# Performance work log

Hardware: AMD Instinct MI355X
Metric: run time of the kernel (lower is better)

## Reference

```python
import jax, jax.numpy as jnp
import numpy as np

_CONTRACTION_EPS = 0.002


def setup_inputs() -> dict:
    key = jax.random.key(0)
    k_u, k_s, k_k = jax.random.split(key, 3)
    B, T, d_in, d_out, d_x = 16, 2048, 512, 512, 512
    u = jax.random.normal(k_u, (B, T, d_in), dtype=jnp.float32)
    state = jnp.zeros((B, d_x), dtype=jnp.float32)
    # mirror init_orthogonal_spectrum: S = I + 0.01 * randn (well-conditioned)
    S = jnp.eye(d_x, dtype=jnp.float32) + 0.01 * jax.random.normal(k_s, (d_x, d_x), dtype=jnp.float32)
    K_raw = jax.random.normal(k_k, (d_x + d_out, d_x + d_in), dtype=jnp.float32)
    log_gamma = jnp.array(0.0, dtype=jnp.float32)  # gamma = 1.0
    return {"u": u, "state": state, "S": S, "K_raw": K_raw, "log_gamma": log_gamma}


def _ssm_matrices(S, K_raw, log_gamma, d_x):
    # contraction: K = K_raw / (sigma_max(K_raw) + eps)
    sigma = jnp.maximum(jnp.linalg.svd(K_raw, compute_uv=False)[0], 1e-5)
    K = K_raw / (sigma + _CONTRACTION_EPS)
    K11 = K[:d_x, :d_x]
    K12 = K[:d_x, d_x:]
    K21 = K[d_x:, :d_x]
    K22 = K[d_x:, d_x:]
    Sinv = jnp.linalg.inv(S)
    gamma = jnp.exp(log_gamma)
    A = Sinv @ K11 @ S
    Bm = gamma * (Sinv @ K12)
    C = K21 @ S
    D = gamma * K22
    return A, Bm, C, D


def reference(u, state, S, K_raw, log_gamma):
    # u: (B, T, d_in), state: (B, d_x)
    d_x = state.shape[1]
    A, Bm, C, D = _ssm_matrices(S, K_raw, log_gamma, d_x)
    At, Bt = A.T, Bm.T

    def step(x, u_t):
        # x_{t+1} = x A^T + u_t B^T ; emit pre-update state x_t
        x_next = x @ At + u_t @ Bt
        return x_next, x

    x_last, pre = jax.lax.scan(step, state, jnp.swapaxes(u, 0, 1))
    pre = jnp.swapaxes(pre, 0, 1)                      # (B, T, d_x) = states[:, :-1]
    states = jnp.concatenate([pre, x_last[:, None, :]], axis=1)  # (B, T+1, d_x)
    # y_t = C x_t + D u_t, vectorized over time
    output = pre @ C.T + u @ D.T                       # (B, T, d_out)
    return output, states
```

## Files before the change

kernel.cpp:

```cpp
#include <hip/hip_runtime.h>
#include <string.h>

typedef _Float16 f16x8 __attribute__((ext_vector_type(8)));
typedef _Float16 f16x4 __attribute__((ext_vector_type(4)));
typedef __fp16   hf2   __attribute__((ext_vector_type(2)));
typedef float    f32x4 __attribute__((ext_vector_type(4)));

struct Addr { long hi; long lo; int sh; int msk; };

__device__ __forceinline__ long raddr(const Addr a, int r) {
  return ((long)(r >> a.sh)) * a.hi + ((long)(r & a.msk)) * a.lo;
}

struct GP {
  int M, N, K1, K2;
  const float* A1; Addr a1;
  const float* A2; Addr a2;
  const _Float16* Bh; int ldbh;
  const float* scale;
  float alpha;
  const float* E1; Addr e1; float beta;
  float* C1; Addr c1;
  _Float16* C1h; int ldh;
  float* C2; Addr c2;
  const float* E2; Addr e2;
  const float* fin;
  float* fout;
};

struct GPB { GP g[10]; };

__device__ __forceinline__ f16x4 pk4s(f32x4 v, float ss) {
  hf2 lo = __builtin_amdgcn_cvt_pkrtz(v[0] * ss, v[1] * ss);
  hf2 hi = __builtin_amdgcn_cvt_pkrtz(v[2] * ss, v[3] * ss);
  f16x4 h;
  h[0] = (_Float16)lo[0]; h[1] = (_Float16)lo[1];
  h[2] = (_Float16)hi[0]; h[3] = (_Float16)hi[1];
  return h;
}

template<int BM, bool DEEP>
__device__ __forceinline__ void gemm_body(const GP& p) {
  constexpr int BN = BM;
  constexpr int WT = BM / 2;
  constexpr int FM = WT / 16;
  constexpr int NAQ = BM / 32;
  constexpr int NBH = BN / 64;
  __shared__ _Float16 As[BM * 40];
  __shared__ _Float16 Bs[BN * 40];
  __shared__ float red[256];
  const int tid = threadIdx.x;
  const int nbn = (p.N + BN - 1) / BN;
  const int nbm = (p.M + BM - 1) / BM;
  if ((int)blockIdx.x >= nbm * nbn) return;
  int bm, bn;
  {
    const int bid = blockIdx.x;
    if ((nbm & 7) == 0) {
      bm = (bid & 7) + ((bid >> 3) / nbn) * 8;
      bn = (bid >> 3) % nbn;
    } else {
      bm = bid / nbn; bn = bid - bm * nbn;
    }
  }
  const int m0 = bm * BM, n0 = bn * BN;

  float sscale = 1.0f;
  if (p.fin) {
    red[tid] = p.fin[tid];
    __syncthreads();
    for (int st = 128; st > 0; st >>= 1) {
      if (tid < st) red[tid] += red[tid + st];
      __syncthreads();
    }
    sscale = 1.0f / sqrtf(red[0]);
    __syncthreads();
  }
  float alpha = p.alpha;
  if (p.scale) alpha *= p.scale[0];
  if (p.fin) alpha *= sscale;

  const int w = tid >> 6, l = tid & 63;
  const int wm = w >> 1, wn = w & 1;
  const int lr = l & 15, lg = l >> 4;

  f32x4 acc[FM][FM];
  #pragma unroll
  for (int m = 0; m < FM; ++m)
    #pragma unroll
    for (int n = 0; n < FM; ++n) acc[m][n] = {0.f, 0.f, 0.f, 0.f};

  const int Kt = p.K1 + p.K2;

  f32x4 aR0[NAQ], aR1[NAQ];
  f16x8 b2R0[NBH], b2R1[NBH];

  auto loadT = [&](int k0, f32x4* aR, f16x8* b2R) {
    const float* Ab; Addr aa; long kl;
    if (k0 < p.K1) { Ab = p.A1; aa = p.a1; kl = k0; }
    else           { Ab = p.A2; aa = p.a2; kl = (long)k0 - p.K1; }
    #pragma unroll
    for (int i = 0; i < NAQ; ++i) {
      const int gq = tid + (i << 8);
      const int ar_ = gq >> 3, kq = gq & 7;
      f32x4 v = {0.f, 0.f, 0.f, 0.f};
      if (m0 + ar_ < p.M) v = *(const f32x4*)(Ab + raddr(aa, m0 + ar_) + kl + kq * 4);
      aR[i] = v;
    }
    #pragma unroll
    for (int i = 0; i < NBH; ++i) {
      const int row = (tid >> 2) + i * 64;
      b2R[i] = *(const f16x8*)(p.Bh + (long)(n0 + row) * p.ldbh + k0 + (tid & 3) * 8);
    }
  };
  auto storeLDS = [&](const f32x4* aR, const f16x8* b2R) {
    #pragma unroll
    for (int i = 0; i < NAQ; ++i) {
      const int gq = tid + (i << 8);
      const int ar_ = gq >> 3, kq = gq & 7;
      *(f16x4*)&As[ar_ * 40 + kq * 4] = pk4s(aR[i], sscale);
    }
    #pragma unroll
    for (int i = 0; i < NBH; ++i) {
      const int row = (tid >> 2) + i * 64;
      *(f16x8*)&Bs[row * 40 + (tid & 3) * 8] = b2R[i];
    }
  };
  auto compute = [&]() {
    f16x8 a[FM], b[FM];
    #pragma unroll
    for (int m = 0; m < FM; ++m)
      a[m] = *(const f16x8*)&As[(wm * WT + m * 16 + lr) * 40 + lg * 8];
    #pragma unroll
    for (int n = 0; n < FM; ++n)
      b[n] = *(const f16x8*)&Bs[(wn * WT + n * 16 + lr) * 40 + lg * 8];
    #pragma unroll
    for (int m = 0; m < FM; ++m)
      #pragma unroll
      for (int n = 0; n < FM; ++n)
        acc[m][n] = __builtin_amdgcn_mfma_f32_16x16x32_f16(a[m], b[n], acc[m][n], 0, 0, 0);
  };

  if constexpr (DEEP) {
    f32x4 aRC[NAQ];
    f16x8 bRC[NBH];
    loadT(0, aR0, b2R0);
    if (Kt > 32) loadT(32, aR1, b2R1);
    for (int k0 = 0; k0 < Kt; k0 += 32) {
      if (k0 + 64 < Kt) loadT(k0 + 64, aRC, bRC);
      storeLDS(aR0, b2R0);
      __syncthreads();
      compute();
      __syncthreads();
      #pragma unroll
      for (int i = 0; i < NAQ; ++i) aR0[i] = aR1[i];
      #pragma unroll
      for (int i = 0; i < NBH; ++i) b2R0[i] = b2R1[i];
      #pragma unroll
      for (int i = 0; i < NAQ; ++i) aR1[i] = aRC[i];
      #pragma unroll
      for (int i = 0; i < NBH; ++i) b2R1[i] = bRC[i];
    }
  } else {
    loadT(0, aR0, b2R0);
    for (int k0 = 0; k0 < Kt; k0 += 64) {
      storeLDS(aR0, b2R0);
      __syncthreads();
      loadT(k0 + 32, aR1, b2R1);
      compute();
      __syncthreads();
      storeLDS(aR1, b2R1);
      __syncthreads();
      if (k0 + 64 < Kt) loadT(k0 + 64, aR0, b2R0);
      compute();
      __syncthreads();
    }
  }

  float ssq = 0.0f;
  #pragma unroll
  for (int m = 0; m < FM; ++m) {
    #pragma unroll
    for (int n = 0; n < FM; ++n) {
      #pragma unroll
      for (int rr = 0; rr < 4; ++rr) {
        const int ro = m0 + wm * WT + m * 16 + lg * 4 + rr;
        const int no = n0 + wn * WT + n * 16 + lr;
        if (ro < p.M) {
          float val = alpha * acc[m][n][rr];
          float o1 = val;
          if (p.E1) o1 += p.beta * p.E1[raddr(p.e1, ro) + no];
          if (p.C1) p.C1[raddr(p.c1, ro) + no] = o1;
          if (p.C1h) p.C1h[(long)no * p.ldh + ro] = (_Float16)o1;
          if (p.C2) p.C2[raddr(p.c2, ro) + no] = val + p.E2[raddr(p.e2, ro) + no];
          ssq += val * val;
        }
      }
    }
  }
  if (p.fout) {
    __syncthreads();
    red[tid] = ssq;
    __syncthreads();
    for (int st = 128; st > 0; st >>= 1) {
      if (tid < st) red[tid] += red[tid + st];
      __syncthreads();
    }
    if (tid == 0) p.fout[blockIdx.x] = red[0];
  }
}

__global__ __launch_bounds__(256) void gemm_u64(GPB pb)  { gemm_body<64, true>(pb.g[blockIdx.y]); }
__global__ __launch_bounds__(256) void gemm_u128(GPB pb) { gemm_body<128, false>(pb.g[blockIdx.y]); }

__global__ void prep1_k(const float* S, const float* Kr, const float* st0,
                        float* Krt, _Float16* KrH, float* St, float* Xa,
                        _Float16* XaH, float* Za,
                        float* K11u, float* K12u, _Float16* K21uH) {
  const int op = blockIdx.y;
  const int tx = threadIdx.x, ty = threadIdx.y;
  const int lid = ty * 32 + tx;
  if (op == 4) {
    if (blockIdx.x >= 256) return;
    const int base = (blockIdx.x * 256 + lid) * 4;
    #pragma unroll
    for (int q = 0; q < 4; ++q) {
      const int e = base + q;
      const int i = e >> 9, j = e & 511;
      XaH[e] = (_Float16)(((i == j) ? 2.0f : 0.0f) - S[(long)i * 512 + j]);
    }
    return;
  }
  if (op == 5) {
    if (blockIdx.x >= 32) return;
    const int idx = blockIdx.x * 256 + lid;
    const int b = idx >> 9, j = idx & 511;
    Za[(long)b * 262144 + j] = st0[idx];
    return;
  }
  if (op == 8) {
    if (blockIdx.x >= 256) return;
    const int base = (blockIdx.x * 256 + lid) * 4;
    #pragma unroll
    for (int q = 0; q < 4; ++q) {
      const int e = base + q;
      const int n = e >> 9, k = e & 511;
      K21uH[e] = (_Float16)Kr[(long)(512 + n) * 1024 + k];
    }
    return;
  }
  __shared__ float t[32][33];
  if (op <= 1) {
    if (blockIdx.x >= 1024) return;
    const int bx = blockIdx.x & 31, by = blockIdx.x >> 5;
    const long I0 = (long)bx * 32, J0 = (long)by * 32;
    #pragma unroll
    for (int k = 0; k < 4; ++k)
      t[ty * 4 + k][tx] = Kr[(J0 + ty * 4 + k) * 1024 + I0 + tx];
    __syncthreads();
    #pragma unroll
    for (int k = 0; k < 4; ++k) {
      const long i = I0 + ty * 4 + k, j = J0 + tx;
      if (op == 0) Krt[i * 1024 + j] = t[tx][ty * 4 + k];
      else         KrH[i * 1024 + j] = (_Float16)t[tx][ty * 4 + k];
    }
  } else {
    if (blockIdx.x >= 256) return;
    const int bx = blockIdx.x & 15, by = blockIdx.x >> 4;
    const long I0 = (long)bx * 32, J0 = (long)by * 32;
    const float* src;
    long ld, coff;
    if (op == 6) { src = Kr; ld = 1024; coff = 0; }
    else if (op == 7) { src = Kr; ld = 1024; coff = 512; }
    else { src = S; ld = 512; coff = 0; }
    #pragma unroll
    for (int k = 0; k < 4; ++k)
      t[ty * 4 + k][tx] = src[(J0 + ty * 4 + k) * ld + coff + I0 + tx];
    __syncthreads();
    #pragma unroll
    for (int k = 0; k < 4; ++k) {
      const long i = I0 + ty * 4 + k, j = J0 + tx;
      if (op == 2) St[i * 512 + j] = t[tx][ty * 4 + k];
      else if (op == 3) Xa[i * 512 + j] = ((i == j) ? 2.0f : 0.0f) - t[tx][ty * 4 + k];
      else if (op == 6) K11u[i * 512 + j] = t[tx][ty * 4 + k];
      else K12u[i * 512 + j] = t[tx][ty * 4 + k];
    }
  }
}

__global__ void prep2_k(const float* Kr, const float* sc, _Float16* ABstH,
                        _Float16* StackH, const _Float16* BtuH,
                        _Float16* CtDtH, float* APf2) {
  const int op = blockIdx.y;
  const int lid = threadIdx.y * 32 + threadIdx.x;
  const float invk = sc[0], gik = sc[2];
  const float ik2 = invk * invk, ik2g = ik2 * sc[1];
  if (op == 0) {
    if (blockIdx.x >= 512) return;
    const int base = (blockIdx.x * 256 + lid) * 4;
    #pragma unroll
    for (int q = 0; q < 4; ++q) {
      const int e = base + q;
      const int n = e >> 10, c = e & 1023;
      if (c < 512) ABstH[e] = (_Float16)((float)ABstH[e] * invk);
      else ABstH[e] = (_Float16)(gik * (float)BtuH[(long)n * 512 + (c - 512)]);
    }
  } else if (op == 1) {
    if (blockIdx.x >= 768) return;
    const int base = (blockIdx.x * 256 + lid) * 4;
    #pragma unroll
    for (int q = 0; q < 4; ++q) {
      const int e = base + q;
      const int n = e / 1536, c = e - n * 1536;
      float v;
      if (c < 512) v = (float)StackH[e] * ik2;
      else if (c < 1024) v = (float)StackH[e] * ik2g;
      else v = gik * (float)BtuH[(long)n * 512 + (c - 1024)];
      StackH[e] = (_Float16)v;
    }
  } else if (op == 2) {
    if (blockIdx.x >= 512) return;
    const int base = (blockIdx.x * 256 + lid) * 4;
    #pragma unroll
    for (int q = 0; q < 4; ++q) {
      const int e = base + q;
      const int n = e >> 10, c = e & 1023;
      if (c < 512) CtDtH[e] = (_Float16)((float)CtDtH[e] * invk);
      else CtDtH[e] = (_Float16)(gik * Kr[(long)(512 + n) * 1024 + 512 + (c - 512)]);
    }
  } else {
    if (blockIdx.x >= 256) return;
    const int base = (blockIdx.x * 256 + lid) * 4;
    #pragma unroll
    for (int q = 0; q < 4; ++q) APf2[base + q] *= ik2;
  }
}

__global__ void scalar_k(const float* P, int nsq, const float* lg, float* sc) {
  __shared__ float red[256];
  __shared__ float sv[16];
  const int tid = threadIdx.x;
  for (int k = 0; k <= nsq; ++k) {
    red[tid] = P[k * 256 + tid];
    __syncthreads();
    for (int st = 128; st > 0; st >>= 1) {
      if (tid < st) red[tid] += red[tid + st];
      __syncthreads();
    }
    if (tid == 0) sv[k] = red[0];
    __syncthreads();
  }
  if (tid != 0) return;
  double lnl = 0.0, wgt = 1.0;
  for (int k = 0; k <= nsq; ++k) {
    double sk = sqrt((double)sv[k]);
    lnl += wgt * log(sk);
    if (k < nsq) wgt *= 0.5;
  }
  double sigma = exp(0.5 * lnl);
  if (sigma < 1e-5) sigma = 1e-5;
  const double invk = 1.0 / (sigma + 0.002);
  const double g = exp((double)lg[0]);
  sc[0] = (float)invk;
  sc[1] = (float)g;
  sc[2] = (float)(g * invk);
}

static inline Addr lin(long stride) {
  Addr a; a.hi = 0; a.lo = stride; a.sh = 20; a.msk = 0xFFFFF; return a;
}
static inline Addr two(int sh, long hi, int msk, long lo) {
  Addr a; a.hi = hi; a.lo = lo; a.sh = sh; a.msk = msk; return a;
}
static inline GP gp0() {
  GP p; memset(&p, 0, sizeof(p)); p.alpha = 1.0f; p.beta = 1.0f; return p;
}

extern "C" void kernel_launch(void* const* d_in, const int* in_sizes, int n_in,
                              void* d_out, int out_size, void* d_ws, size_t ws_size,
                              hipStream_t stream) {
  (void)in_sizes; (void)n_in; (void)out_size; (void)ws_size;
  const float* u    = (const float*)d_in[0];
  const float* st0  = (const float*)d_in[1];
  const float* S    = (const float*)d_in[2];
  const float* Kr   = (const float*)d_in[3];
  const float* lgam = (const float*)d_in[4];

  float* outp   = (float*)d_out;
  float* states = outp + (long)16 * 2048 * 512;
  float* ws = (float*)d_ws;

  const int NSQ = 8;
  float* sc = ws;
  float* P  = ws + 64;
  float* base = ws + 3456;

  float* Krt = base;
  _Float16* MbH = (_Float16*)base;
  float* Ma  = base + 1048576;
  float* Mb  = base + 2097152;
  _Float16* CtDtH  = (_Float16*)(ws + 3149248);
  _Float16* MaH    = (_Float16*)(ws + 3419584);
  _Float16* StackH = (_Float16*)(ws + 3943872);
  _Float16* zerosH = (_Float16*)(ws + 4337088);

  float* Za  = outp;
  float* Zb  = outp + 4194304;
  float* APb = outp + 8388608;
  float* Tb  = outp + 10223616;
  float* K11u = Tb;
  float* K12u = Tb + 262144;
  float* AtU  = Tb + 524288;
  float* BtU  = Tb + 786432;
  _Float16* h16   = (_Float16*)(outp + 12320768);
  _Float16* ABstH = h16;
  _Float16* APH_  = h16 + 524288;
  _Float16* TmH_  = h16 + 2097152;
  _Float16* XaH   = h16 + 4194304;
  _Float16* XbH   = XaH + 262144;
  _Float16* YnH   = XbH + 262144;
  _Float16* WH    = YnH + 262144;
  _Float16* K21uH = WH + 262144;
  _Float16* KrH   = K21uH + 262144;
  _Float16* BtuH  = h16 + 6553600;
  float* St = outp + 15728640;
  float* Xa = outp + 15990784;
  float* Xb = outp + 16252928;
  float* Yn = outp + 16515072;

  auto APf = [&](int j) -> float* {
    return APb + (long)(j - 2) * 262144;
  };
  auto APHp = [&](int j) -> const _Float16* {
    if (j == 1) return ABstH;
    if (j == 2) return StackH;
    return APH_ + (long)(j - 3) * 262144;
  };
  auto APHl = [&](int j) { return (j == 1) ? 1024 : ((j == 2) ? 1536 : 512); };
  auto Tmf = [&](int k) -> float* { return (k == 0) ? APf(8) : Tb + (long)(k - 1) * 262144; };
  auto TmH = [&](int k) -> _Float16* {
    return (k == 0) ? (_Float16*)APHp(8) : TmH_ + (long)(k - 1) * 262144;
  };

  auto launch64 = [&](const GP* gs, int nb) {
    GPB pb; memset(&pb, 0, sizeof(pb));
    int mx = 0;
    for (int i = 0; i < nb; ++i) {
      pb.g[i] = gs[i];
      int b = ((gs[i].M + 63) / 64) * ((gs[i].N + 63) / 64);
      if (b > mx) mx = b;
    }
    gemm_u64<<<dim3(mx, nb), dim3(256), 0, stream>>>(pb);
  };
  auto launch128 = [&](const GP* gs, int nb) {
    GPB pb; memset(&pb, 0, sizeof(pb));
    int mx = 0;
    for (int i = 0; i < nb; ++i) {
      pb.g[i] = gs[i];
      int b = ((gs[i].M + 127) / 128) * ((gs[i].N + 127) / 128);
      if (b > mx) mx = b;
    }
    gemm_u128<<<dim3(mx, nb), dim3(256), 0, stream>>>(pb);
  };

  auto mmh = [&](const float* A, const _Float16* Bh, int ldbh,
                 float* C, _Float16* Ch, int ldh) {
    GP g = gp0(); g.M = 512; g.N = 512; g.K1 = 512;
    g.A1 = A; g.a1 = lin(512);
    g.Bh = Bh; g.ldbh = ldbh;
    g.C1 = C; g.c1 = lin(512);
    g.C1h = Ch; g.ldh = ldh;
    return g;
  };
  auto cpGP = [&](const float* src, Addr sa, float* dst, Addr da, int M) {
    GP g = gp0(); g.M = M; g.N = 512; g.K1 = 64;
    g.A1 = src; g.a1 = sa;
    g.Bh = zerosH; g.ldbh = 64;
    g.E1 = src; g.e1 = sa; g.beta = 1.0f;
    g.C1 = dst; g.c1 = da;
    return g;
  };

  hipMemsetAsync(zerosH, 0, 512 * 64 * sizeof(_Float16), stream);
  prep1_k<<<dim3(1024, 9), dim3(32, 8), 0, stream>>>(S, Kr, st0, Krt, KrH,
                                                     St, Xa, XaH, Za,
                                                     K11u, K12u, K21uH);

  {
    GP gs[2];
    gs[0] = gp0();
    gs[0].M = 1024; gs[0].N = 1024; gs[0].K1 = 1024;
    gs[0].A1 = Krt; gs[0].a1 = lin(1024);
    gs[0].Bh = KrH; gs[0].ldbh = 1024;
    gs[0].C1 = Ma; gs[0].c1 = lin(1024);
    gs[0].C1h = MaH; gs[0].ldh = 1024;
    gs[0].fout = P;
    gs[1] = mmh(St, XaH, 512, Yn, YnH, 512);
    launch64(gs, 2);
  }
  for (int k = 1; k <= NSQ; ++k) {
    const bool odd = (k % 2 == 1);
    float* cur = odd ? Ma : Mb;
    float* nxt = odd ? Mb : Ma;
    _Float16* curH = odd ? MaH : MbH;
    _Float16* nxtH = odd ? MbH : MaH;
    GP gs[3];
    gs[0] = gp0();
    gs[0].M = 1024; gs[0].N = 1024; gs[0].K1 = 1024;
    gs[0].A1 = cur; gs[0].a1 = lin(1024);
    gs[0].Bh = curH; gs[0].ldbh = 1024;
    gs[0].C1 = nxt; gs[0].c1 = lin(1024);
    gs[0].C1h = nxtH; gs[0].ldh = 1024;
    gs[0].fin = P + (long)(k - 1) * 256;
    gs[0].fout = P + (long)k * 256;
    int nb = 1;
    if (k <= 5) {
      if (odd) {
        float* cx = (k == 1 || k == 5) ? Xa : Xb;
        float* nx = (k == 1 || k == 5) ? Xb : Xa;
        _Float16* nxH = (k == 1 || k == 5) ? XbH : XaH;
        GP h = mmh(cx, YnH, 512, nx, nxH, 512);
        h.alpha = -1.0f; h.E1 = cx; h.e1 = lin(512); h.beta = 2.0f;
        gs[nb++] = h;
      } else {
        _Float16* cxH = (k == 2) ? XbH : XaH;
        gs[nb++] = mmh(St, cxH, 512, Yn, YnH, 512);
      }
    } else if (k == 6) {
      gs[nb++] = mmh(K11u, XbH, 512, nullptr, WH, 512);
      gs[nb++] = mmh(St, K21uH, 512, nullptr, CtDtH, 1024);
    } else if (k == 7) {
      gs[nb++] = mmh(St, WH, 512, AtU, ABstH, 1024);
      gs[nb++] = mmh(K12u, XbH, 512, BtU, BtuH, 512);
    } else {
      gs[nb++] = mmh(AtU, ABstH, 1024, APf(2), StackH, 1536);
      gs[nb++] = mmh(BtU, ABstH, 1024, nullptr, StackH + 512, 1536);
    }
    launch64(gs, nb);
  }
  scalar_k<<<1, 256, 0, stream>>>(P, NSQ, lgam, sc);
  prep2_k<<<dim3(768, 4), dim3(32, 8), 0, stream>>>(Kr, sc, ABstH, StackH,
                                                    BtuH, CtDtH, APf(2));

  const Addr A_u8   = two(8, 1048576, 255, 4096);
  const Addr A_s8   = two(8, 1049088, 255, 4096);
  const Addr A_z    = two(8, 262144, 255, 512);
  const Addr A_srow = two(11, 1049088, 2047, 512);

  for (int j = 2; j <= 8; j += 2) {
    GP gs[5];
    int nb = 0;
    GP m = gp0();
    m.M = 4096; m.N = 512;
    if (j == 2) {
      m.K1 = 1024; m.A1 = u; m.a1 = A_u8;
      m.Bh = StackH + 512; m.ldbh = 1536;
    } else {
      m.K1 = 512; m.A1 = states + (long)(j - 2) * 512; m.a1 = A_s8;
      m.K2 = 1024; m.A2 = u + (long)(j - 2) * 512; m.a2 = A_u8;
      m.Bh = StackH; m.ldbh = 1536;
    }
    if (j == 8) { m.C1 = Za + 512; m.c1 = A_z; }
    else { m.C1 = states + (long)j * 512; m.c1 = A_s8; }
    gs[nb++] = m;
    if (j == 2) {
      gs[nb++] = mmh(APf(2), ABstH, 1024, APf(3), APH_ + 0, 512);
      gs[nb++] = mmh(APf(2), StackH, 1536, APf(4), APH_ + 262144, 512);
    } else if (j == 4) {
      for (int i = 1; i <= 4; ++i)
        gs[nb++] = mmh(APf(4), APHp(i), APHl(i), APf(4 + i),
                       APH_ + (long)(i + 1) * 262144, 512);
    } else if (j == 6) {
      gs[nb++] = mmh(Tmf(0), TmH(0), 512, Tmf(1), TmH(1), 512);
    } else {
      gs[nb++] = mmh(Tmf(1), TmH(1), 512, Tmf(2), TmH(2), 512);
    }
    launch64(gs, nb);
  }

  for (int k = 0; k <= 2; ++k) {
    const int s = 1 << k;
    float* Zs = (k % 2 == 0) ? Za : Zb;
    float* Zd = (k % 2 == 0) ? Zb : Za;
    GP gs[7];
    int nb = 0;
    GP m = gp0();
    m.M = 4096; m.N = 512; m.K1 = 512;
    m.A1 = Zs; m.a1 = A_z;
    m.Bh = TmH(k); m.ldbh = 512;
    m.E1 = Zs + (long)s * 512; m.e1 = A_z; m.beta = 1.0f;
    m.C1 = Zd + (long)s * 512; m.c1 = A_z;
    gs[nb++] = m;
    const Addr lowA = two(k, 262144, s - 1, 512);
    gs[nb++] = cpGP(Zs, lowA, Zd, lowA, 16 * s);
    if (k == 0) {
      for (int j = 1; j <= 7; j += 2) {
        GP g = gp0();
        g.M = 4096; g.N = 512;
        if (j == 1) {
          g.K1 = 512; g.A1 = u; g.a1 = A_u8;
          g.Bh = ABstH + 512; g.ldbh = 1024;
        } else {
          g.K1 = 512; g.A1 = states + (long)(j - 1) * 512; g.a1 = A_s8;
          g.K2 = 512; g.A2 = u + (long)(j - 1) * 512; g.a2 = A_u8;
          g.Bh = ABstH; g.ldbh = 1024;
        }
        g.C1 = states + (long)j * 512; g.c1 = A_s8;
        gs[nb++] = g;
      }
    }
    launch64(gs, nb);
  }
  float* Zf = Zb;

  {
    GP gs[9];
    for (int j = 1; j <= 7; ++j) {
      GP g = gp0();
      g.M = 4096; g.N = 512; g.K1 = 512;
      g.A1 = Zf; g.a1 = A_z;
      g.Bh = APHp(j); g.ldbh = APHl(j);
      g.C2 = states + (long)j * 512; g.c2 = A_s8;
      g.E2 = states + (long)j * 512; g.e2 = A_s8;
      gs[j - 1] = g;
    }
    gs[7] = cpGP(Zf, A_z, states, A_s8, 4096);
    gs[8] = cpGP(Zf + (long)256 * 512, lin(262144),
                 states + (long)2048 * 512, lin(1049088), 16);
    launch128(gs, 9);
  }

  {
    GP g = gp0();
    g.M = 32768; g.N = 512;
    g.K1 = 512; g.A1 = states; g.a1 = A_srow;
    g.K2 = 512; g.A2 = u; g.a2 = lin(512);
    g.Bh = CtDtH; g.ldbh = 1024;
    g.C1 = outp; g.c1 = lin(512);
    launch128(&g, 1);
  }
}
```

Baseline: 581.6 us.

## Restructure chunked scan schedule with 4-step stack and fold scalar kernel into prep2

Adds a 4-step stacked input matrix (A^3B, A^2B, AB, B scaled by powers of the contraction factor) so the intra-chunk state recurrence jumps directly from states[0] to states[4] and then to the chunk end. It regroups the batched GEMM launches across the log-depth Z scan so independent state GEMMs run alongside the scan stages, cutting the number of dependent launches. It also merges the scalar reduction kernel into prep2 (every block recomputes sigma) and replaces a memset with a prep1 op. In exchange there is more redundant reduction work per block, a larger K=2048 GEMM, and buffer aliasing (BtAtU on Tb, Stack4H over Xa) that must not collide with live data.

```diff
diff --git a/kernel.cpp b/kernel.cpp
--- a/kernel.cpp
+++ b/kernel.cpp
@@ -216,7 +216,8 @@
 __global__ void prep1_k(const float* S, const float* Kr, const float* st0,
                         float* Krt, _Float16* KrH, float* St, float* Xa,
                         _Float16* XaH, float* Za,
-                        float* K11u, float* K12u, _Float16* K21uH) {
+                        float* K11u, float* K12u, _Float16* K21uH,
+                        _Float16* zerosH) {
   const int op = blockIdx.y;
   const int tx = threadIdx.x, ty = threadIdx.y;
   const int lid = ty * 32 + tx;
@@ -247,6 +248,12 @@
       const int n = e >> 9, k = e & 511;
       K21uH[e] = (_Float16)Kr[(long)(512 + n) * 1024 + k];
     }
+    return;
+  }
+  if (op == 9) {
+    if (blockIdx.x >= 32) return;
+    const int base = (blockIdx.x * 256 + lid);
+    *(f16x4*)&zerosH[base * 4] = f16x4{0, 0, 0, 0};
     return;
   }
   __shared__ float t[32][33];
@@ -288,13 +295,39 @@
   }
 }
 
-__global__ void prep2_k(const float* Kr, const float* sc, _Float16* ABstH,
-                        _Float16* StackH, const _Float16* BtuH,
-                        _Float16* CtDtH, float* APf2) {
+__global__ void prep2_k(const float* Kr, const float* P, const float* lg,
+                        _Float16* ABstH, _Float16* StackH,
+                        const _Float16* BtuH, _Float16* CtDtH, float* APf2,
+                        _Float16* Stack4H, const float* BtAtU) {
+  __shared__ float red[256];
+  __shared__ float sv[9];
+  const int lid = threadIdx.y * 32 + threadIdx.x;
+  for (int k = 0; k < 9; ++k) {
+    red[lid] = P[k * 256 + lid];
+    __syncthreads();
+    for (int st = 128; st > 0; st >>= 1) {
+      if (lid < st) red[lid] += red[lid + st];
+      __syncthreads();
+    }
+    if (lid == 0) sv[k] = red[0];
+    __syncthreads();
+  }
+  double lnl = 0.0, wgt = 1.0;
+  for (int k = 0; k < 9; ++k) {
+    lnl += wgt * log(sqrt((double)sv[k]));
+    if (k < 8) wgt *= 0.5;
+  }
+  double sigma = exp(0.5 * lnl);
+  if (sigma < 1e-5) sigma = 1e-5;
+  const float invk = (float)(1.0 / (sigma + 0.002));
+  const float gma  = (float)exp((double)lg[0]);
+  const float gik  = gma * invk;
+  const float ik2  = invk * invk;
+  const float ik2g = ik2 * gma;
+  const float ik3g = ik2 * invk * gma;
+  const float ik4g = ik2 * ik2 * gma;
+
   const int op = blockIdx.y;
-  const int lid = threadIdx.y * 32 + threadIdx.x;
-  const float invk = sc[0], gik = sc[2];
-  const float ik2 = invk * invk, ik2g = ik2 * sc[1];
   if (op == 0) {
     if (blockIdx.x >= 512) return;
     const int base = (blockIdx.x * 256 + lid) * 4;
@@ -328,42 +361,27 @@
       if (c < 512) CtDtH[e] = (_Float16)((float)CtDtH[e] * invk);
       else CtDtH[e] = (_Float16)(gik * Kr[(long)(512 + n) * 1024 + 512 + (c - 512)]);
     }
-  } else {
+  } else if (op == 3) {
     if (blockIdx.x >= 256) return;
     const int base = (blockIdx.x * 256 + lid) * 4;
     #pragma unroll
     for (int q = 0; q < 4; ++q) APf2[base + q] *= ik2;
-  }
-}
-
-__global__ void scalar_k(const float* P, int nsq, const float* lg, float* sc) {
-  __shared__ float red[256];
-  __shared__ float sv[16];
-  const int tid = threadIdx.x;
-  for (int k = 0; k <= nsq; ++k) {
-    red[tid] = P[k * 256 + tid];
-    __syncthreads();
-    for (int st = 128; st > 0; st >>= 1) {
-      if (tid < st) red[tid] += red[tid + st];
-      __syncthreads();
-    }
-    if (tid == 0) sv[k] = red[0];
-    __syncthreads();
-  }
-  if (tid != 0) return;
-  double lnl = 0.0, wgt = 1.0;
-  for (int k = 0; k <= nsq; ++k) {
-    double sk = sqrt((double)sv[k]);
-    lnl += wgt * log(sk);
-    if (k < nsq) wgt *= 0.5;
-  }
-  double sigma = exp(0.5 * lnl);
-  if (sigma < 1e-5) sigma = 1e-5;
-  const double invk = 1.0 / (sigma + 0.002);
-  const double g = exp((double)lg[0]);
-  sc[0] = (float)invk;
-  sc[1] = (float)g;
-  sc[2] = (float)(g * invk);
+  } else {
+    if (blockIdx.x >= 1024) return;
+    const int base = (blockIdx.x * 256 + lid) * 4;
+    #pragma unroll
+    for (int q = 0; q < 4; ++q) {
+      const int e = base + q;
+      const int n = e >> 11, c = e & 2047;
+      _Float16* dst = &Stack4H[(long)n * 2560 + 512 + c];
+      float v;
+      if (c < 512) v = (float)*dst * ik4g;
+      else if (c < 1024) v = (float)*dst * ik3g;
+      else if (c < 1536) v = ik2g * BtAtU[(long)(c - 1024) * 512 + n];
+      else v = gik * (float)BtuH[(long)n * 512 + (c - 1536)];
+      *dst = (_Float16)v;
+    }
+  }
 }
 
 static inline Addr lin(long stride) {
@@ -391,7 +409,6 @@
   float* ws = (float*)d_ws;
 
   const int NSQ = 8;
-  float* sc = ws;
   float* P  = ws + 64;
   float* base = ws + 3456;
 
@@ -408,10 +425,11 @@
   float* Zb  = outp + 4194304;
   float* APb = outp + 8388608;
   float* Tb  = outp + 10223616;
-  float* K11u = Tb;
-  float* K12u = Tb + 262144;
-  float* AtU  = Tb + 524288;
-  float* BtU  = Tb + 786432;
+  float* K11u  = Tb;
+  float* K12u  = Tb + 262144;
+  float* AtU   = Tb + 524288;
+  float* BtU   = Tb + 786432;
+  float* BtAtU = Tb;
   _Float16* h16   = (_Float16*)(outp + 12320768);
   _Float16* ABstH = h16;
   _Float16* APH_  = h16 + 524288;
@@ -427,6 +445,7 @@
   float* Xa = outp + 15990784;
   float* Xb = outp + 16252928;
   float* Yn = outp + 16515072;
+  _Float16* Stack4H = (_Float16*)(outp + 15990784);
 
   auto APf = [&](int j) -> float* {
     return APb + (long)(j - 2) * 262144;
@@ -434,9 +453,12 @@
   auto APHp = [&](int j) -> const _Float16* {
     if (j == 1) return ABstH;
     if (j == 2) return StackH;
+    if (j == 4) return Stack4H;
     return APH_ + (long)(j - 3) * 262144;
   };
-  auto APHl = [&](int j) { return (j == 1) ? 1024 : ((j == 2) ? 1536 : 512); };
+  auto APHl = [&](int j) {
+    return (j == 1) ? 1024 : ((j == 2) ? 1536 : ((j == 4) ? 2560 : 512));
+  };
   auto Tmf = [&](int k) -> float* { return (k == 0) ? APf(8) : Tb + (long)(k - 1) * 262144; };
   auto TmH = [&](int k) -> _Float16* {
     return (k == 0) ? (_Float16*)APHp(8) : TmH_ + (long)(k - 1) * 262144;
@@ -481,10 +503,9 @@
     return g;
   };
 
-  hipMemsetAsync(zerosH, 0, 512 * 64 * sizeof(_Float16), stream);
-  prep1_k<<<dim3(1024, 9), dim3(32, 8), 0, stream>>>(S, Kr, st0, Krt, KrH,
-                                                     St, Xa, XaH, Za,
-                                                     K11u, K12u, K21uH);
+  prep1_k<<<dim3(1024, 10), dim3(32, 8), 0, stream>>>(S, Kr, st0, Krt, KrH,
+                                                      St, Xa, XaH, Za,
+                                                      K11u, K12u, K21uH, zerosH);
 
   {
     GP gs[2];
@@ -534,55 +555,57 @@
       gs[nb++] = mmh(K12u, XbH, 512, BtU, BtuH, 512);
     } else {
       gs[nb++] = mmh(AtU, ABstH, 1024, APf(2), StackH, 1536);
-      gs[nb++] = mmh(BtU, ABstH, 1024, nullptr, StackH + 512, 1536);
+      gs[nb++] = mmh(BtU, ABstH, 1024, BtAtU, StackH + 512, 1536);
     }
     launch64(gs, nb);
   }
-  scalar_k<<<1, 256, 0, stream>>>(P, NSQ, lgam, sc);
-  prep2_k<<<dim3(768, 4), dim3(32, 8), 0, stream>>>(Kr, sc, ABstH, StackH,
-                                                    BtuH, CtDtH, APf(2));
+
+  {
+    GP gs[2];
+    gs[0] = mmh(BtAtU, ABstH, 1024, nullptr, Stack4H + 1024, 2560);
+    gs[1] = mmh(BtAtU, StackH, 1536, nullptr, Stack4H + 512, 2560);
+    launch64(gs, 2);
+  }
+  prep2_k<<<dim3(1024, 5), dim3(32, 8), 0, stream>>>(Kr, P, lgam, ABstH, StackH,
+                                                     BtuH, CtDtH, APf(2),
+                                                     Stack4H, BtAtU);
 
   const Addr A_u8   = two(8, 1048576, 255, 4096);
   const Addr A_s8   = two(8, 1049088, 255, 4096);
   const Addr A_z    = two(8, 262144, 255, 512);
   const Addr A_srow = two(11, 1049088, 2047, 512);
 
-  for (int j = 2; j <= 8; j += 2) {
+  {
+    GP gs[3];
+    gs[0] = gp0();
+    gs[0].M = 4096; gs[0].N = 512;
+    gs[0].K1 = 2048; gs[0].A1 = u; gs[0].a1 = A_u8;
+    gs[0].Bh = Stack4H + 512; gs[0].ldbh = 2560;
+    gs[0].C1 = states + (long)4 * 512; gs[0].c1 = A_s8;
+    gs[1] = mmh(APf(2), ABstH, 1024, nullptr, APH_ + 0, 512);
+    gs[2] = mmh(APf(2), StackH, 1536, APf(4), Stack4H, 2560);
+    launch64(gs, 3);
+  }
+  {
     GP gs[5];
-    int nb = 0;
-    GP m = gp0();
-    m.M = 4096; m.N = 512;
-    if (j == 2) {
-      m.K1 = 1024; m.A1 = u; m.a1 = A_u8;
-      m.Bh = StackH + 512; m.ldbh = 1536;
-    } else {
-      m.K1 = 512; m.A1 = states + (long)(j - 2) * 512; m.a1 = A_s8;
-      m.K2 = 1024; m.A2 = u + (long)(j - 2) * 512; m.a2 = A_u8;
-      m.Bh = StackH; m.ldbh = 1536;
-    }
-    if (j == 8) { m.C1 = Za + 512; m.c1 = A_z; }
-    else { m.C1 = states + (long)j * 512; m.c1 = A_s8; }
-    gs[nb++] = m;
-    if (j == 2) {
-      gs[nb++] = mmh(APf(2), ABstH, 1024, APf(3), APH_ + 0, 512);
-      gs[nb++] = mmh(APf(2), StackH, 1536, APf(4), APH_ + 262144, 512);
-    } else if (j == 4) {
-      for (int i = 1; i <= 4; ++i)
-        gs[nb++] = mmh(APf(4), APHp(i), APHl(i), APf(4 + i),
-                       APH_ + (long)(i + 1) * 262144, 512);
-    } else if (j == 6) {
-      gs[nb++] = mmh(Tmf(0), TmH(0), 512, Tmf(1), TmH(1), 512);
-    } else {
-      gs[nb++] = mmh(Tmf(1), TmH(1), 512, Tmf(2), TmH(2), 512);
-    }
-    launch64(gs, nb);
+    gs[0] = gp0();
+    gs[0].M = 4096; gs[0].N = 512;
+    gs[0].K1 = 512; gs[0].A1 = states + (long)4 * 512; gs[0].a1 = A_s8;
+    gs[0].K2 = 2048; gs[0].A2 = u + (long)4 * 512; gs[0].a2 = A_u8;
+    gs[0].Bh = Stack4H; gs[0].ldbh = 2560;
+    gs[0].C1 = Za + 512; gs[0].c1 = A_z;
+    gs[1] = mmh(APf(4), ABstH, 1024, nullptr, APH_ + 2 * 262144, 512);
+    gs[2] = mmh(APf(4), StackH, 1536, nullptr, APH_ + 3 * 262144, 512);
+    gs[3] = mmh(APf(4), APH_ + 0, 512, nullptr, APH_ + 4 * 262144, 512);
+    gs[4] = mmh(APf(4), Stack4H, 2560, APf(8), APH_ + 5 * 262144, 512);
+    launch64(gs, 5);
   }
 
   for (int k = 0; k <= 2; ++k) {
     const int s = 1 << k;
     float* Zs = (k % 2 == 0) ? Za : Zb;
     float* Zd = (k % 2 == 0) ? Zb : Za;
-    GP gs[7];
+    GP gs[8];
     int nb = 0;
     GP m = gp0();
     m.M = 4096; m.N = 512; m.K1 = 512;
@@ -594,20 +617,55 @@
     const Addr lowA = two(k, 262144, s - 1, 512);
     gs[nb++] = cpGP(Zs, lowA, Zd, lowA, 16 * s);
     if (k == 0) {
-      for (int j = 1; j <= 7; j += 2) {
-        GP g = gp0();
-        g.M = 4096; g.N = 512;
-        if (j == 1) {
-          g.K1 = 512; g.A1 = u; g.a1 = A_u8;
-          g.Bh = ABstH + 512; g.ldbh = 1024;
-        } else {
-          g.K1 = 512; g.A1 = states + (long)(j - 1) * 512; g.a1 = A_s8;
-          g.K2 = 512; g.A2 = u + (long)(j - 1) * 512; g.a2 = A_u8;
-          g.Bh = ABstH; g.ldbh = 1024;
-        }
-        g.C1 = states + (long)j * 512; g.c1 = A_s8;
+      {
+        GP g = gp0(); g.M = 4096; g.N = 512;
+        g.K1 = 512; g.A1 = u; g.a1 = A_u8;
+        g.Bh = ABstH + 512; g.ldbh = 1024;
+        g.C1 = states + (long)1 * 512; g.c1 = A_s8;
         gs[nb++] = g;
       }
+      {
+        GP g = gp0(); g.M = 4096; g.N = 512;
+        g.K1 = 1024; g.A1 = u; g.a1 = A_u8;
+        g.Bh = StackH + 512; g.ldbh = 1536;
+        g.C1 = states + (long)2 * 512; g.c1 = A_s8;
+        gs[nb++] = g;
+      }
+      {
+        GP g = gp0(); g.M = 4096; g.N = 512;
+        g.K1 = 512; g.A1 = states + (long)4 * 512; g.a1 = A_s8;
+        g.K2 = 512; g.A2 = u + (long)4 * 512; g.a2 = A_u8;
+        g.Bh = ABstH; g.ldbh = 1024;
+        g.C1 = states + (long)5 * 512; g.c1 = A_s8;
+        gs[nb++] = g;
+      }
+      {
+        GP g = gp0(); g.M = 4096; g.N = 512;
+        g.K1 = 512; g.A1 = states + (long)4 * 512; g.a1 = A_s8;
+        g.K2 = 1024; g.A2 = u + (long)4 * 512; g.a2 = A_u8;
+        g.Bh = StackH; g.ldbh = 1536;
+        g.C1 = states + (long)6 * 512; g.c1 = A_s8;
+        gs[nb++] = g;
+      }
+      gs[nb++] = mmh(Tmf(0), TmH(0), 512, Tmf(1), TmH(1), 512);
+    } else if (k == 1) {
+      {
+        GP g = gp0(); g.M = 4096; g.N = 512;
+        g.K1 = 512; g.A1 = states + (long)2 * 512; g.a1 = A_s8;
+        g.K2 = 512; g.A2 = u + (long)2 * 512; g.a2 = A_u8;
+        g.Bh = ABstH; g.ldbh = 1024;
+        g.C1 = states + (long)3 * 512; g.c1 = A_s8;
+        gs[nb++] = g;
+      }
+      {
+        GP g = gp0(); g.M = 4096; g.N = 512;
+        g.K1 = 512; g.A1 = states + (long)6 * 512; g.a1 = A_s8;
+        g.K2 = 512; g.A2 = u + (long)6 * 512; g.a2 = A_u8;
+        g.Bh = ABstH; g.ldbh = 1024;
+        g.C1 = states + (long)7 * 512; g.c1 = A_s8;
+        gs[nb++] = g;
+      }
+      gs[nb++] = mmh(Tmf(1), TmH(1), 512, nullptr, TmH(2), 512);
     }
     launch64(gs, nb);
   }
```

After: 633.8 us. +9.0%, slower.
